# Kernel optimization log

Measured on AMD Instinct MI355X. Metric: run time of the kernel, lower is better.

## Reference

```python
import jax, jax.numpy as jnp
import numpy as np

L = 16          # hash-grid levels (opt.L)
F = 2           # features per level
N_MIN = 16      # base resolution
T = 1 << 19     # hashmap size per level (log2_T = 19, bound == 1)
BOUND = 1.0
B = float(np.exp(np.log(512.0 / 16.0) / (L - 1)))  # per-level scale
PRIMES = np.array([1, 2654435761, 805459861], dtype=np.uint32)
# 8 corner offsets of the trilinear cell, in {0,1}^3
OFFS = np.array([[i, j, k] for i in (0, 1) for j in (0, 1) for k in (0, 1)], dtype=np.float32)


def hash_grid_encode(xn, tables):
    """xn: [N,3] in [0,1]; tables: [L,T,F]. Returns [N, L*F]."""
    offs_f = jnp.asarray(OFFS)                      # [8,3] float
    offs_u = jnp.asarray(OFFS.astype(np.uint32))    # [8,3] uint32
    primes = jnp.asarray(PRIMES)
    feats = []
    for l in range(L):
        res = int(np.floor(N_MIN * B ** l))
        pos = xn * res                              # [N,3]
        pf = jnp.minimum(jnp.floor(pos), float(res - 1))
        frac = pos - pf                             # [N,3], grads flow to x
        base = pf.astype(jnp.uint32)                # [N,3]
        corners = base[:, None, :] + offs_u[None]   # [N,8,3]
        if (res + 1) ** 3 <= T:
            # grid fits in table: coherent dense indexing (tcnn behavior)
            stride = jnp.asarray(np.array([1, res + 1, (res + 1) ** 2], dtype=np.uint32))
            idx = (corners * stride).sum(-1)        # [N,8]
        else:
            h = corners * primes                    # uint32 wraps (mod 2^32)
            idx = (h[..., 0] ^ h[..., 1] ^ h[..., 2]) & jnp.uint32(T - 1)
        vals = tables[l, idx.astype(jnp.int32)]     # [N,8,F] gather
        w = jnp.prod(jnp.where(offs_f[None] > 0, frac[:, None, :], 1.0 - frac[:, None, :]), axis=-1)  # [N,8]
        feats.append(jnp.einsum('nc,ncf->nf', w, vals))
    return jnp.concatenate(feats, axis=-1)          # [N, L*F]


def _wn(v, g):
    # torch weight_norm, dim=0: per-output-row normalization
    return g[:, None] * v / jnp.linalg.norm(v, axis=1, keepdims=True)


def setup_inputs() -> dict:
    key = jax.random.key(0)
    k = jax.random.split(key, 4)
    N = 2097152
    x = jax.random.uniform(k[0], (N, 3), jnp.float32, -BOUND, BOUND)
    tables = jax.random.normal(k[1], (L, T, F), jnp.float32) * 1e-2
    v1 = jax.random.normal(k[2], (64, L * F), jnp.float32) * (1.0 / np.sqrt(L * F))
    g1 = jnp.ones((64,), jnp.float32)
    b1 = jnp.zeros((64,), jnp.float32)
    v2 = jax.random.normal(k[3], (3, 64), jnp.float32) * (1.0 / 8.0)
    g2 = jnp.ones((3,), jnp.float32)
    b2 = jnp.zeros((3,), jnp.float32)
    return {"x": x, "tables": tables, "v1": v1, "g1": g1, "b1": b1,
            "v2": v2, "g2": g2, "b2": b2}


def reference(x, tables, v1, g1, b1, v2, g2, b2):
    xn = (x + BOUND) / (2.0 * BOUND)                # map to [0,1]
    h = hash_grid_encode(xn, tables)                # [N, 32]
    h1 = jax.nn.relu(h @ _wn(v1, g1).T + b1)        # [N, 64]
    out = jnp.tanh(h1 @ _wn(v2, g2).T + b2)         # [N, 3]
    return out
```

## Files before the change

### kernel.cpp

```cpp
#include <hip/hip_runtime.h>
#include <math.h>

#define LVL 16
#define TBL (1u << 19)
#define PR1 2654435761u
#define PR2 805459861u
#define NDENSE 7
#define NHASH 9
#define NXY 5

typedef __attribute__((ext_vector_type(4))) float f4;
typedef __attribute__((ext_vector_type(4))) unsigned u4;
typedef __attribute__((ext_vector_type(8))) short bf16x8;
typedef __attribute__((ext_vector_type(4))) float f32x4;

union FragU { unsigned u[4]; bf16x8 v; };

struct EncParams {
    float resf[LVL];
    float resm1[LVL];
    unsigned s1[LVL];
    unsigned s2[LVL];
    unsigned dense_mask;
};

struct FinalParams {
    float resf[NDENSE];
    float resm1[NDENSE];
    unsigned s1[NDENSE];
    unsigned s2[NDENSE];
    unsigned off1_5, off1_6;
};

struct XYBuild { unsigned S[NXY]; unsigned s1[NXY]; };

static __device__ __forceinline__ unsigned f2bf(float f) {
    unsigned u = __float_as_uint(f);
    u += 0x7FFFu + ((u >> 16) & 1u);
    return u >> 16;
}
static __device__ __forceinline__ float bf_lo(unsigned p) { return __uint_as_float(p << 16); }
static __device__ __forceinline__ float bf_hi(unsigned p) { return __uint_as_float(p & 0xFFFF0000u); }

static __device__ __forceinline__ float fast_tanh(float v) {
    v = fminf(fmaxf(v, -10.f), 10.f);
    float e = __expf(2.0f * v);
    return __fdividef(e - 1.0f, e + 1.0f);
}

static __device__ __forceinline__ void gather8_sc0(const unsigned* __restrict__ tb,
                                                   const unsigned* off, unsigned* val)
{
    asm volatile(
        "global_load_dword %0, %8, %16 sc0\n\t"
        "global_load_dword %1, %9, %16 sc0\n\t"
        "global_load_dword %2, %10, %16 sc0\n\t"
        "global_load_dword %3, %11, %16 sc0\n\t"
        "global_load_dword %4, %12, %16 sc0\n\t"
        "global_load_dword %5, %13, %16 sc0\n\t"
        "global_load_dword %6, %14, %16 sc0\n\t"
        "global_load_dword %7, %15, %16 sc0\n\t"
        "s_waitcnt vmcnt(0)"
        : "=&v"(val[0]), "=&v"(val[1]), "=&v"(val[2]), "=&v"(val[3]),
          "=&v"(val[4]), "=&v"(val[5]), "=&v"(val[6]), "=&v"(val[7])
        : "v"(off[0]), "v"(off[1]), "v"(off[2]), "v"(off[3]),
          "v"(off[4]), "v"(off[5]), "v"(off[6]), "v"(off[7]),
          "s"(tb)
        : "memory");
}

static __device__ __forceinline__ void gather4x2_sc0(const unsigned* __restrict__ tb,
                                                     const unsigned* off,
                                                     unsigned long long* val)
{
    asm volatile(
        "global_load_dwordx2 %0, %4, %8 sc0\n\t"
        "global_load_dwordx2 %1, %5, %8 sc0\n\t"
        "global_load_dwordx2 %2, %6, %8 sc0\n\t"
        "global_load_dwordx2 %3, %7, %8 sc0\n\t"
        "s_waitcnt vmcnt(0)"
        : "=&v"(val[0]), "=&v"(val[1]), "=&v"(val[2]), "=&v"(val[3])
        : "v"(off[0]), "v"(off[1]), "v"(off[2]), "v"(off[3]),
          "s"(tb)
        : "memory");
}

static __device__ __forceinline__ void gather8x2_sc0(const unsigned* __restrict__ tb,
                                                     const unsigned* off,
                                                     unsigned long long* val)
{
    asm volatile(
        "global_load_dwordx2 %0, %8, %16 sc0\n\t"
        "global_load_dwordx2 %1, %9, %16 sc0\n\t"
        "global_load_dwordx2 %2, %10, %16 sc0\n\t"
        "global_load_dwordx2 %3, %11, %16 sc0\n\t"
        "global_load_dwordx2 %4, %12, %16 sc0\n\t"
        "global_load_dwordx2 %5, %13, %16 sc0\n\t"
        "global_load_dwordx2 %6, %14, %16 sc0\n\t"
        "global_load_dwordx2 %7, %15, %16 sc0\n\t"
        "s_waitcnt vmcnt(0)"
        : "=&v"(val[0]), "=&v"(val[1]), "=&v"(val[2]), "=&v"(val[3]),
          "=&v"(val[4]), "=&v"(val[5]), "=&v"(val[6]), "=&v"(val[7])
        : "v"(off[0]), "v"(off[1]), "v"(off[2]), "v"(off[3]),
          "v"(off[4]), "v"(off[5]), "v"(off[6]), "v"(off[7]),
          "s"(tb)
        : "memory");
}

static __device__ __forceinline__ void gather10x4_sc0(const unsigned* __restrict__ tb,
                                                      const unsigned* off, u4* val)
{
    asm volatile(
        "global_load_dwordx4 %0, %10, %20 sc0\n\t"
        "global_load_dwordx4 %1, %11, %20 sc0\n\t"
        "global_load_dwordx4 %2, %12, %20 sc0\n\t"
        "global_load_dwordx4 %3, %13, %20 sc0\n\t"
        "global_load_dwordx4 %4, %14, %20 sc0\n\t"
        "global_load_dwordx4 %5, %15, %20 sc0\n\t"
        "global_load_dwordx4 %6, %16, %20 sc0\n\t"
        "global_load_dwordx4 %7, %17, %20 sc0\n\t"
        "global_load_dwordx4 %8, %18, %20 sc0\n\t"
        "global_load_dwordx4 %9, %19, %20 sc0\n\t"
        "s_waitcnt vmcnt(0)"
        : "=&v"(val[0]), "=&v"(val[1]), "=&v"(val[2]), "=&v"(val[3]), "=&v"(val[4]),
          "=&v"(val[5]), "=&v"(val[6]), "=&v"(val[7]), "=&v"(val[8]), "=&v"(val[9])
        : "v"(off[0]), "v"(off[1]), "v"(off[2]), "v"(off[3]), "v"(off[4]),
          "v"(off[5]), "v"(off[6]), "v"(off[7]), "v"(off[8]), "v"(off[9]),
          "s"(tb)
        : "memory");
}

__global__ __launch_bounds__(256)
void prep_weights(const float* __restrict__ v1, const float* __restrict__ g1,
                  const float* __restrict__ v2, const float* __restrict__ g2,
                  float* __restrict__ ws)
{
    int t = threadIdx.x;
    if (t < 64) {
        float row[32];
        float s = 0.f;
        for (int i = 0; i < 32; ++i) { row[i] = v1[t * 32 + i]; s += row[i] * row[i]; }
        float sc = g1[t] / sqrtf(s);
        unsigned* wbf = (unsigned*)ws + 2304;
        for (int i = 0; i < 32; ++i) ws[t * 32 + i] = row[i] * sc;
        for (int w = 0; w < 16; ++w)
            wbf[t * 16 + w] = (f2bf(row[2 * w + 1] * sc) << 16) | f2bf(row[2 * w] * sc);
    } else if (t < 67) {
        int r = t - 64;
        float s = 0.f;
        for (int i = 0; i < 64; ++i) { float v = v2[r * 64 + i]; s += v * v; }
        float scale = g2[r] / sqrtf(s);
        for (int i = 0; i < 64; ++i) ws[2048 + r * 64 + i] = v2[r * 64 + i] * scale;
    }
}

__global__ __launch_bounds__(256)
void convert_tables(const float* __restrict__ src, unsigned* __restrict__ dst, int npairs)
{
    int j = blockIdx.x * 256 + threadIdx.x;
    if (j >= npairs) return;
    f4 v = __builtin_nontemporal_load((const f4*)src + j);
    unsigned lo = (f2bf(v.y) << 16) | f2bf(v.x);
    unsigned hi = (f2bf(v.w) << 16) | f2bf(v.z);
    unsigned long long o = ((unsigned long long)hi << 32) | lo;
    __builtin_nontemporal_store(o, (unsigned long long*)dst + j);
}

__global__ __launch_bounds__(256)
void build_xy(const float* __restrict__ tables, unsigned* __restrict__ region, XYBuild xb)
{
    int l = blockIdx.y;
    unsigned e = blockIdx.x * 256 + threadIdx.x;
    unsigned S = xb.S[l];
    if (e >= S) return;
    unsigned s1 = xb.s1[l];
    const float* src = tables + (size_t)l * TBL * 2;
    unsigned e10 = (e + 1u < S) ? e + 1u : e;
    unsigned e01 = (e + s1 < S) ? e + s1 : e;
    unsigned e11 = (e + s1 + 1u < S) ? e + s1 + 1u : e;
    u4 o;
    o[0] = (f2bf(src[2 * e   + 1]) << 16) | f2bf(src[2 * e]);
    o[1] = (f2bf(src[2 * e10 + 1]) << 16) | f2bf(src[2 * e10]);
    o[2] = (f2bf(src[2 * e01 + 1]) << 16) | f2bf(src[2 * e01]);
    o[3] = (f2bf(src[2 * e11 + 1]) << 16) | f2bf(src[2 * e11]);
    *(u4*)(region + (size_t)l * TBL + 4u * e) = o;
}

__global__ __launch_bounds__(256)
void build_pair1(unsigned* __restrict__ region, unsigned src_dw, unsigned dst_dw, unsigned n)
{
    unsigned e = blockIdx.x * 256 + threadIdx.x;
    if (e + 1 < n)
        region[dst_dw + e] = region[src_dw + e + 1];
}

__global__ __launch_bounds__(256, 4)
void encode_hash4(const float* __restrict__ x, const unsigned* __restrict__ tb,
                  unsigned* __restrict__ hout, int N, float rf, float rm1)
{
    int j = blockIdx.x * 256 + threadIdx.x;
    int i0 = 4 * j;
    if (i0 >= N) return;

    if (i0 + 4 <= N) {
        const f4* xp = (const f4*)(x + (size_t)3 * i0);
        f4 q0 = __builtin_nontemporal_load(xp);
        f4 q1 = __builtin_nontemporal_load(xp + 1);
        f4 q2 = __builtin_nontemporal_load(xp + 2);
        float n0[4], n1[4], n2[4];
        n0[0] = (q0.x + 1.f) * 0.5f; n1[0] = (q0.y + 1.f) * 0.5f; n2[0] = (q0.z + 1.f) * 0.5f;
        n0[1] = (q0.w + 1.f) * 0.5f; n1[1] = (q1.x + 1.f) * 0.5f; n2[1] = (q1.y + 1.f) * 0.5f;
        n0[2] = (q1.z + 1.f) * 0.5f; n1[2] = (q1.w + 1.f) * 0.5f; n2[2] = (q2.x + 1.f) * 0.5f;
        n0[3] = (q2.y + 1.f) * 0.5f; n1[3] = (q2.z + 1.f) * 0.5f; n2[3] = (q2.w + 1.f) * 0.5f;

        unsigned o[4];
#pragma unroll
        for (int p = 0; p < 4; ++p) {
            float a0 = n0[p] * rf, a1 = n1[p] * rf, a2 = n2[p] * rf;
            float w0 = fminf(floorf(a0), rm1);
            float w1 = fminf(floorf(a1), rm1);
            float w2 = fminf(floorf(a2), rm1);
            float f0 = a0 - w0, f1 = a1 - w1, f2 = a2 - w2;
            unsigned c0 = (unsigned)w0;
            unsigned hx0 = c0, hx1 = c0 + 1u;
            unsigned hy0 = (unsigned)w1 * PR1, hy1 = hy0 + PR1;
            unsigned hz0 = (unsigned)w2 * PR2, hz1 = hz0 + PR2;

            float acc0, acc1;
            if (!(c0 & 1u)) {
                unsigned pb[4], qq[4];
#pragma unroll
                for (int jj = 0; jj < 4; ++jj) {
                    unsigned hyv = (jj & 2) ? hy1 : hy0;
                    unsigned hzv = (jj & 1) ? hz1 : hz0;
                    unsigned idx0 = (hx0 ^ hyv ^ hzv) & (TBL - 1u);
                    qq[jj] = idx0 & 1u;
                    pb[jj] = (idx0 & ~1u) << 2;
                }
                unsigned long long pv[4];
                gather4x2_sc0(tb, pb, pv);
                float wx1 = f0, wx0 = 1.f - f0;
                acc0 = 0.f; acc1 = 0.f;
#pragma unroll
                for (int jj = 0; jj < 4; ++jj) {
                    unsigned lo = (unsigned)pv[jj];
                    unsigned hi = (unsigned)(pv[jj] >> 32);
                    unsigned x0 = qq[jj] ? hi : lo;
                    unsigned x1 = qq[jj] ? lo : hi;
                    float wyz = ((jj & 2) ? f1 : 1.f - f1) * ((jj & 1) ? f2 : 1.f - f2);
                    acc0 = fmaf(wyz, fmaf(wx0, bf_lo(x0), wx1 * bf_lo(x1)), acc0);
                    acc1 = fmaf(wyz, fmaf(wx0, bf_hi(x0), wx1 * bf_hi(x1)), acc1);
                }
            } else {
                unsigned off[8];
#pragma unroll
                for (int c = 0; c < 8; ++c) {
                    unsigned hx = (c & 4) ? hx1 : hx0;
                    unsigned hy = (c & 2) ? hy1 : hy0;
                    unsigned hz = (c & 1) ? hz1 : hz0;
                    off[c] = ((hx ^ hy ^ hz) & (TBL - 1u)) << 2;
                }
                unsigned v[8];
                gather8_sc0(tb, off, v);
                acc0 = 0.f; acc1 = 0.f;
#pragma unroll
                for (int c = 0; c < 8; ++c) {
                    float w = ((c & 4) ? f0 : 1.f - f0) *
                              ((c & 2) ? f1 : 1.f - f1) *
                              ((c & 1) ? f2 : 1.f - f2);
                    acc0 = fmaf(w, bf_lo(v[c]), acc0);
                    acc1 = fmaf(w, bf_hi(v[c]), acc1);
                }
            }
            o[p] = (f2bf(acc1) << 16) | f2bf(acc0);
        }
        u4 ov = {o[0], o[1], o[2], o[3]};
        __builtin_nontemporal_store(ov, (u4*)(hout + i0));
    } else {
        for (int i = i0; i < N; ++i) {
            float xn0 = (x[3 * i + 0] + 1.0f) * 0.5f;
            float xn1 = (x[3 * i + 1] + 1.0f) * 0.5f;
            float xn2 = (x[3 * i + 2] + 1.0f) * 0.5f;
            float p0 = xn0 * rf, p1 = xn1 * rf, p2 = xn2 * rf;
            float pf0 = fminf(floorf(p0), rm1), pf1 = fminf(floorf(p1), rm1), pf2 = fminf(floorf(p2), rm1);
            float fg0 = p0 - pf0, fg1 = p1 - pf1, fg2 = p2 - pf2;
            unsigned hx0 = (unsigned)pf0, hx1 = hx0 + 1u;
            unsigned hy0 = (unsigned)pf1 * PR1, hy1 = hy0 + PR1;
            unsigned hz0 = (unsigned)pf2 * PR2, hz1 = hz0 + PR2;
            float a0 = 0.f, a1 = 0.f;
#pragma unroll
            for (int c = 0; c < 8; ++c) {
                unsigned hxv = (c & 4) ? hx1 : hx0;
                unsigned hyv = (c & 2) ? hy1 : hy0;
                unsigned hzv = (c & 1) ? hz1 : hz0;
                unsigned vv = tb[(hxv ^ hyv ^ hzv) & (TBL - 1u)];
                float w = ((c & 4) ? fg0 : 1.f - fg0) * ((c & 2) ? fg1 : 1.f - fg1) * ((c & 1) ? fg2 : 1.f - fg2);
                a0 = fmaf(w, bf_lo(vv), a0);
                a1 = fmaf(w, bf_hi(vv), a1);
            }
            hout[i] = (f2bf(a1) << 16) | f2bf(a0);
        }
    }
}

__global__ __launch_bounds__(256, 4)
void final_mfma(const float* __restrict__ x, const unsigned* __restrict__ tb,
                const unsigned* __restrict__ hbuf, const unsigned* __restrict__ w1bf,
                const float* __restrict__ b1, const float* __restrict__ w2,
                const float* __restrict__ b2, float* __restrict__ out,
                int N, FinalParams dp)
{
    __shared__ unsigned lds[256 * 20];
    int tid = threadIdx.x;
    int i = blockIdx.x * 256 + tid;

    unsigned hp[NHASH];
#pragma unroll
    for (int l = 0; l < NHASH; ++l)
        hp[l] = __builtin_nontemporal_load(hbuf + (size_t)l * N + i);

    float xn0 = (__builtin_nontemporal_load(x + 3 * i + 0) + 1.0f) * 0.5f;
    float xn1 = (__builtin_nontemporal_load(x + 3 * i + 1) + 1.0f) * 0.5f;
    float xn2 = (__builtin_nontemporal_load(x + 3 * i + 2) + 1.0f) * 0.5f;

    float fr[NDENSE][3];
    unsigned bb[NDENSE];
#pragma unroll
    for (int l = 0; l < NDENSE; ++l) {
        float rf = dp.resf[l];
        float p0 = xn0 * rf, p1 = xn1 * rf, p2 = xn2 * rf;
        float pf0 = fminf(floorf(p0), dp.resm1[l]);
        float pf1 = fminf(floorf(p1), dp.resm1[l]);
        float pf2 = fminf(floorf(p2), dp.resm1[l]);
        fr[l][0] = p0 - pf0; fr[l][1] = p1 - pf1; fr[l][2] = p2 - pf2;
        bb[l] = (unsigned)pf0 + (unsigned)pf1 * dp.s1[l] + (unsigned)pf2 * dp.s2[l];
    }

    unsigned offxy[2 * NXY];
#pragma unroll
    for (int l = 0; l < NXY; ++l) {
        unsigned base = l * (TBL * 4u);
        offxy[2 * l + 0] = base + bb[l] * 16u;
        offxy[2 * l + 1] = base + (bb[l] + dp.s2[l]) * 16u;
    }
    unsigned off56[8];
#pragma unroll
    for (int h = 0; h < 2; ++h) {
        int l = 5 + h;
        unsigned base0 = l * (TBL * 4u);
        unsigned base1 = h ? dp.off1_6 : dp.off1_5;
        unsigned s1 = dp.s1[l], s2 = dp.s2[l];
#pragma unroll
        for (int jj = 0; jj < 4; ++jj) {
            unsigned e = bb[l] + ((jj & 2) ? s1 : 0u) + ((jj & 1) ? s2 : 0u);
            off56[4 * h + jj] = (e & 1u) ? (base1 + ((e - 1u) << 2)) : (base0 + (e << 2));
        }
    }

    unsigned hw[16];
    {
        u4 xv[2 * NXY];
        gather10x4_sc0(tb, offxy, xv);
#pragma unroll
        for (int l = 0; l < NXY; ++l) {
            float wx1 = fr[l][0], wx0 = 1.f - wx1;
            float wy1 = fr[l][1], wy0 = 1.f - wy1;
            float wz1 = fr[l][2];
            float acc0 = 0.f, acc1 = 0.f;
#pragma unroll
            for (int z = 0; z < 2; ++z) {
                u4 e = xv[2 * l + z];
                float wz = z ? wz1 : 1.f - wz1;
                float lo = wy0 * fmaf(wx0, bf_lo(e[0]), wx1 * bf_lo(e[1]))
                         + wy1 * fmaf(wx0, bf_lo(e[2]), wx1 * bf_lo(e[3]));
                float hi = wy0 * fmaf(wx0, bf_hi(e[0]), wx1 * bf_hi(e[1]))
                         + wy1 * fmaf(wx0, bf_hi(e[2]), wx1 * bf_hi(e[3]));
                acc0 = fmaf(wz, lo, acc0);
                acc1 = fmaf(wz, hi, acc1);
            }
            hw[l] = (f2bf(acc1) << 16) | f2bf(acc0);
        }
    }
    {
        unsigned long long pv[8];
        gather8x2_sc0(tb, off56, pv);
#pragma unroll
        for (int h = 0; h < 2; ++h) {
            int l = 5 + h;
            float wx1 = fr[l][0], wx0 = 1.f - wx1;
            float f1v = fr[l][1], f2v = fr[l][2];
            float acc0 = 0.f, acc1 = 0.f;
#pragma unroll
            for (int jj = 0; jj < 4; ++jj) {
                unsigned long long pvv = pv[4 * h + jj];
                unsigned lo = (unsigned)pvv;
                unsigned hi = (unsigned)(pvv >> 32);
                float wyz = ((jj & 2) ? f1v : 1.f - f1v) * ((jj & 1) ? f2v : 1.f - f2v);
                acc0 = fmaf(wyz, fmaf(wx0, bf_lo(lo), wx1 * bf_lo(hi)), acc0);
                acc1 = fmaf(wyz, fmaf(wx0, bf_hi(lo), wx1 * bf_hi(hi)), acc1);
            }
            hw[l] = (f2bf(acc1) << 16) | f2bf(acc0);
        }
    }
#pragma unroll
    for (int l = 0; l < NHASH; ++l) hw[NDENSE + l] = hp[l];

    unsigned* row = &lds[tid * 20];
#pragma unroll
    for (int c = 0; c < 4; ++c)
        *(uint4*)(row + 4 * c) = make_uint4(hw[4 * c], hw[4 * c + 1], hw[4 * c + 2], hw[4 * c + 3]);

    __syncthreads();

    int lane = tid & 63;
    int wv   = tid >> 6;
    int l16  = lane & 15;
    int lhi  = lane >> 4;

    bf16x8 bfr[4];
#pragma unroll
    for (int t = 0; t < 4; ++t) {
        const unsigned* p = w1bf + (t * 16 + l16) * 16 + lhi * 4;
        FragU u;
        u.u[0] = p[0]; u.u[1] = p[1]; u.u[2] = p[2]; u.u[3] = p[3];
        bfr[t] = u.v;
    }
    float b1v[4];
#pragma unroll
    for (int t = 0; t < 4; ++t) b1v[t] = b1[t * 16 + l16];
    float w2v[3][4];
#pragma unroll
    for (int jj = 0; jj < 3; ++jj)
#pragma unroll
        for (int t = 0; t < 4; ++t) w2v[jj][t] = w2[jj * 64 + t * 16 + l16];
    float bias2 = (l16 < 3) ? b2[l16] : 0.f;

#pragma unroll
    for (int g = 0; g < 4; ++g) {
        const unsigned* rp = &lds[(wv * 64 + g * 16 + l16) * 20 + lhi * 4];
        FragU u;
        u.u[0] = rp[0]; u.u[1] = rp[1]; u.u[2] = rp[2]; u.u[3] = rp[3];
        bf16x8 af = u.v;

        f32x4 acc[4];
#pragma unroll
        for (int t = 0; t < 4; ++t) {
            f32x4 z = {0.f, 0.f, 0.f, 0.f};
            acc[t] = __builtin_amdgcn_mfma_f32_16x16x32_bf16(af, bfr[t], z, 0, 0, 0);
        }

#pragma unroll
        for (int r = 0; r < 4; ++r) {
            float p0 = 0.f, p1 = 0.f, p2 = 0.f;
#pragma unroll
            for (int t = 0; t < 4; ++t) {
                float a = fmaxf(acc[t][r] + b1v[t], 0.f);
                p0 = fmaf(a, w2v[0][t], p0);
                p1 = fmaf(a, w2v[1][t], p1);
                p2 = fmaf(a, w2v[2][t], p2);
            }
#pragma unroll
            for (int m = 1; m < 16; m <<= 1) {
                p0 += __shfl_xor(p0, m);
                p1 += __shfl_xor(p1, m);
                p2 += __shfl_xor(p2, m);
            }
            if (l16 < 3) {
                int point = blockIdx.x * 256 + wv * 64 + g * 16 + lhi * 4 + r;
                float v = (l16 == 0) ? p0 : ((l16 == 1) ? p1 : p2);
                out[(size_t)point * 3 + l16] = fast_tanh(v + bias2);
            }
        }
    }
}

__global__ __launch_bounds__(256)
void fused_ngp(const float* __restrict__ x, const float* __restrict__ tables,
               const float* __restrict__ w1, const float* __restrict__ b1,
               const float* __restrict__ w2, const float* __restrict__ b2,
               float* __restrict__ out, int N, EncParams ep)
{
    int i = blockIdx.x * 256 + threadIdx.x;
    if (i >= N) return;

    float xn0 = (x[3 * i + 0] + 1.0f) * 0.5f;
    float xn1 = (x[3 * i + 1] + 1.0f) * 0.5f;
    float xn2 = (x[3 * i + 2] + 1.0f) * 0.5f;

    float h[2 * LVL];

#pragma unroll
    for (int l = 0; l < LVL; ++l) {
        float rf = ep.resf[l];
        float p0 = xn0 * rf, p1 = xn1 * rf, p2 = xn2 * rf;
        float pf0 = fminf(floorf(p0), ep.resm1[l]);
        float pf1 = fminf(floorf(p1), ep.resm1[l]);
        float pf2 = fminf(floorf(p2), ep.resm1[l]);
        float fr0 = p0 - pf0, fr1 = p1 - pf1, fr2 = p2 - pf2;
        unsigned c0 = (unsigned)pf0, c1 = (unsigned)pf1, c2 = (unsigned)pf2;
        const float2* tb = (const float2*)tables + (size_t)l * TBL;

        float acc0 = 0.f, acc1 = 0.f;
        if ((ep.dense_mask >> l) & 1u) {
            unsigned s1 = ep.s1[l], s2 = ep.s2[l];
            unsigned b = c0 + c1 * s1 + c2 * s2;
#pragma unroll
            for (int c = 0; c < 8; ++c) {
                unsigned id = b + ((c & 4) ? 1u : 0u) + ((c & 2) ? s1 : 0u) + ((c & 1) ? s2 : 0u);
                float2 v = tb[id];
                float w = ((c & 4) ? fr0 : 1.f - fr0) * ((c & 2) ? fr1 : 1.f - fr1) * ((c & 1) ? fr2 : 1.f - fr2);
                acc0 = fmaf(w, v.x, acc0);
                acc1 = fmaf(w, v.y, acc1);
            }
        } else {
            unsigned hx0 = c0, hx1 = c0 + 1u;
            unsigned hy0 = c1 * PR1, hy1 = hy0 + PR1;
            unsigned hz0 = c2 * PR2, hz1 = hz0 + PR2;
#pragma unroll
            for (int c = 0; c < 8; ++c) {
                unsigned hx = (c & 4) ? hx1 : hx0;
                unsigned hy = (c & 2) ? hy1 : hy0;
                unsigned hz = (c & 1) ? hz1 : hz0;
                float2 v = tb[(hx ^ hy ^ hz) & (TBL - 1u)];
                float w = ((c & 4) ? fr0 : 1.f - fr0) * ((c & 2) ? fr1 : 1.f - fr1) * ((c & 1) ? fr2 : 1.f - fr2);
                acc0 = fmaf(w, v.x, acc0);
                acc1 = fmaf(w, v.y, acc1);
            }
        }
        h[2 * l + 0] = acc0;
        h[2 * l + 1] = acc1;
    }

    float r0 = b2[0], r1 = b2[1], r2 = b2[2];
    for (int o = 0; o < 64; ++o) {
        float a = b1[o];
#pragma unroll
        for (int k = 0; k < 32; ++k) a = fmaf(h[k], w1[o * 32 + k], a);
        a = fmaxf(a, 0.f);
        r0 = fmaf(a, w2[0 * 64 + o], r0);
        r1 = fmaf(a, w2[1 * 64 + o], r1);
        r2 = fmaf(a, w2[2 * 64 + o], r2);
    }
    out[3 * i + 0] = tanhf(r0);
    out[3 * i + 1] = tanhf(r1);
    out[3 * i + 2] = tanhf(r2);
}

extern "C" void kernel_launch(void* const* d_in, const int* in_sizes, int n_in,
                              void* d_out, int out_size, void* d_ws, size_t ws_size,
                              hipStream_t stream)
{
    const float* x      = (const float*)d_in[0];
    const float* tables = (const float*)d_in[1];
    const float* v1     = (const float*)d_in[2];
    const float* g1     = (const float*)d_in[3];
    const float* b1     = (const float*)d_in[4];
    const float* v2     = (const float*)d_in[5];
    const float* g2     = (const float*)d_in[6];
    const float* b2     = (const float*)d_in[7];
    float* out = (float*)d_out;
    float* ws  = (float*)d_ws;
    int N = in_sizes[0] / 3;

    EncParams ep;
    double Bd = exp(log(512.0 / 16.0) / (double)(LVL - 1));
    unsigned dm = 0;
    int resv[LVL];
    for (int l = 0; l < LVL; ++l) {
        int res = (int)floor(16.0 * pow(Bd, (double)l));
        resv[l] = res;
        ep.resf[l]  = (float)res;
        ep.resm1[l] = (float)(res - 1);
        long long rp1 = (long long)res + 1;
        if (rp1 * rp1 * rp1 <= (long long)TBL) dm |= (1u << l);
        ep.s1[l] = (unsigned)(res + 1);
        ep.s2[l] = (unsigned)((res + 1) * (res + 1));
    }
    ep.dense_mask = dm;

    prep_weights<<<1, 256, 0, stream>>>(v1, g1, v2, g2, ws);

    size_t tb_off_bytes = 16384;
    unsigned S[NDENSE];
    for (int l = 0; l < NDENSE; ++l) {
        unsigned s1 = (unsigned)(resv[l] + 1);
        S[l] = s1 * s1 * s1;
    }
    bool xy_ok = true;
    for (int l = 0; l < NXY; ++l) if (4ull * S[l] > TBL) xy_ok = false;

    unsigned cum_dw = LVL * TBL;
    unsigned off1_5_dw = cum_dw; cum_dw += (S[5] + 3u) & ~1u;
    unsigned off1_6_dw = cum_dw; cum_dw += (S[6] + 3u) & ~1u;
    cum_dw = (cum_dw + 3u) & ~3u;
    size_t h_off_bytes = tb_off_bytes + (size_t)cum_dw * 4;
    size_t need = h_off_bytes + (size_t)NHASH * (size_t)N * 4;

    bool fast = (ws_size >= need) && (dm == 0x7Fu) && (N % 1024 == 0) && xy_ok;
    if (fast) {
        unsigned* tb   = (unsigned*)((char*)d_ws + tb_off_bytes);
        unsigned* hbuf = (unsigned*)((char*)d_ws + h_off_bytes);
        unsigned* w1bf = (unsigned*)ws + 2304;

        int npairs = (int)((size_t)LVL * TBL / 2);
        convert_tables<<<(npairs + 255) / 256, 256, 0, stream>>>(tables, tb, npairs);

        XYBuild xb;
        unsigned maxSxy = 0;
        for (int l = 0; l < NXY; ++l) {
            xb.S[l] = S[l]; xb.s1[l] = ep.s1[l];
            if (S[l] > maxSxy) maxSxy = S[l];
        }
        dim3 xgrid((maxSxy + 255) / 256, NXY);
        build_xy<<<xgrid, 256, 0, stream>>>(tables, tb, xb);

        build_pair1<<<(S[5] + 255) / 256, 256, 0, stream>>>(tb, 5u * TBL, off1_5_dw, S[5]);
        build_pair1<<<(S[6] + 255) / 256, 256, 0, stream>>>(tb, 6u * TBL, off1_6_dw, S[6]);

        int grid4 = N / 1024;
        for (int l = 0; l < NHASH; ++l) {
            int gl = NDENSE + l;
            encode_hash4<<<grid4, 256, 0, stream>>>(
                x, tb + (size_t)gl * TBL, hbuf + (size_t)l * N, N,
                ep.resf[gl], ep.resm1[gl]);
        }

        FinalParams dp;
        for (int l = 0; l < NDENSE; ++l) {
            dp.resf[l] = ep.resf[l]; dp.resm1[l] = ep.resm1[l];
            dp.s1[l] = ep.s1[l];     dp.s2[l] = ep.s2[l];
        }
        dp.off1_5 = off1_5_dw * 4u;
        dp.off1_6 = off1_6_dw * 4u;
        final_mfma<<<N / 256, 256, 0, stream>>>(x, tb, hbuf, w1bf, b1,
                                                ws + 2048, b2, out, N, dp);
    } else {
        fused_ngp<<<(N + 255) / 256, 256, 0, stream>>>(x, tables, ws, b1, ws + 2048, b2, out, N, ep);
    }
}
```

Baseline: 652.3 us.

## Pack all 8 trilinear corners per cell contiguously for dense levels 0-4

Replaces the xy-pair layout, which stored 4 corners per vertex and needed two strided 16-byte gathers per level, with a per-cell layout. Each cell stores all 8 bf16-packed corners in 32 contiguous bytes, so the final kernel reads two adjacent 16-byte chunks. These likely fall in the same cache line, which should cut memory transactions and cache-line traffic for the dense levels. In exchange the preprocessing build writes 32 bytes per cell, roughly twice as much as before, and the in-place xy_ok guard is removed because the cells now live in a separate workspace region.

Result: faster. 630.9 us (-3.3%).

```diff
diff --git a/kernel.cpp b/kernel.cpp
--- a/kernel.cpp
+++ b/kernel.cpp
@@ -29,10 +29,18 @@
     float resm1[NDENSE];
     unsigned s1[NDENSE];
     unsigned s2[NDENSE];
+    unsigned cellbase[NXY];
+    unsigned cres[NXY];
+    unsigned cres2[NXY];
     unsigned off1_5, off1_6;
 };
 
-struct XYBuild { unsigned S[NXY]; unsigned s1[NXY]; };
+struct CellBuild {
+    unsigned nc[NXY];
+    unsigned res[NXY];
+    unsigned s1[NXY], s2[NXY];
+    unsigned dst_dw[NXY];
+};
 
 static __device__ __forceinline__ unsigned f2bf(float f) {
     unsigned u = __float_as_uint(f);
@@ -167,23 +175,27 @@
 }
 
 __global__ __launch_bounds__(256)
-void build_xy(const float* __restrict__ tables, unsigned* __restrict__ region, XYBuild xb)
+void build_cell(const float* __restrict__ tables, unsigned* __restrict__ region, CellBuild cb)
 {
     int l = blockIdx.y;
-    unsigned e = blockIdx.x * 256 + threadIdx.x;
-    unsigned S = xb.S[l];
-    if (e >= S) return;
-    unsigned s1 = xb.s1[l];
+    unsigned c = blockIdx.x * 256 + threadIdx.x;
+    if (c >= cb.nc[l]) return;
+    unsigned res = cb.res[l];
+    unsigned cx = c % res, t = c / res;
+    unsigned cy = t % res, cz = t / res;
+    unsigned s1 = cb.s1[l], s2 = cb.s2[l];
+    unsigned base = cx + cy * s1 + cz * s2;
     const float* src = tables + (size_t)l * TBL * 2;
-    unsigned e10 = (e + 1u < S) ? e + 1u : e;
-    unsigned e01 = (e + s1 < S) ? e + s1 : e;
-    unsigned e11 = (e + s1 + 1u < S) ? e + s1 + 1u : e;
-    u4 o;
-    o[0] = (f2bf(src[2 * e   + 1]) << 16) | f2bf(src[2 * e]);
-    o[1] = (f2bf(src[2 * e10 + 1]) << 16) | f2bf(src[2 * e10]);
-    o[2] = (f2bf(src[2 * e01 + 1]) << 16) | f2bf(src[2 * e01]);
-    o[3] = (f2bf(src[2 * e11 + 1]) << 16) | f2bf(src[2 * e11]);
-    *(u4*)(region + (size_t)l * TBL + 4u * e) = o;
+    unsigned o[8];
+#pragma unroll
+    for (int k = 0; k < 8; ++k) {
+        unsigned e = base + (k & 1u) + ((k >> 1) & 1u) * s1 + (k >> 2) * s2;
+        o[k] = (f2bf(src[2 * e + 1]) << 16) | f2bf(src[2 * e]);
+    }
+    u4* dst = (u4*)(region + cb.dst_dw[l] + 8u * c);
+    u4 o0 = {o[0], o[1], o[2], o[3]};
+    u4 o1 = {o[4], o[5], o[6], o[7]};
+    dst[0] = o0; dst[1] = o1;
 }
 
 __global__ __launch_bounds__(256)
@@ -324,7 +336,7 @@
     float xn2 = (__builtin_nontemporal_load(x + 3 * i + 2) + 1.0f) * 0.5f;
 
     float fr[NDENSE][3];
-    unsigned bb[NDENSE];
+    unsigned cc[NDENSE][3];
 #pragma unroll
     for (int l = 0; l < NDENSE; ++l) {
         float rf = dp.resf[l];
@@ -333,15 +345,16 @@
         float pf1 = fminf(floorf(p1), dp.resm1[l]);
         float pf2 = fminf(floorf(p2), dp.resm1[l]);
         fr[l][0] = p0 - pf0; fr[l][1] = p1 - pf1; fr[l][2] = p2 - pf2;
-        bb[l] = (unsigned)pf0 + (unsigned)pf1 * dp.s1[l] + (unsigned)pf2 * dp.s2[l];
+        cc[l][0] = (unsigned)pf0; cc[l][1] = (unsigned)pf1; cc[l][2] = (unsigned)pf2;
     }
 
     unsigned offxy[2 * NXY];
 #pragma unroll
     for (int l = 0; l < NXY; ++l) {
-        unsigned base = l * (TBL * 4u);
-        offxy[2 * l + 0] = base + bb[l] * 16u;
-        offxy[2 * l + 1] = base + (bb[l] + dp.s2[l]) * 16u;
+        unsigned c = cc[l][0] + cc[l][1] * dp.cres[l] + cc[l][2] * dp.cres2[l];
+        unsigned base = dp.cellbase[l] + c * 32u;
+        offxy[2 * l + 0] = base;
+        offxy[2 * l + 1] = base + 16u;
     }
     unsigned off56[8];
 #pragma unroll
@@ -350,9 +363,10 @@
         unsigned base0 = l * (TBL * 4u);
         unsigned base1 = h ? dp.off1_6 : dp.off1_5;
         unsigned s1 = dp.s1[l], s2 = dp.s2[l];
+        unsigned b = cc[l][0] + cc[l][1] * s1 + cc[l][2] * s2;
 #pragma unroll
         for (int jj = 0; jj < 4; ++jj) {
-            unsigned e = bb[l] + ((jj & 2) ? s1 : 0u) + ((jj & 1) ? s2 : 0u);
+            unsigned e = b + ((jj & 2) ? s1 : 0u) + ((jj & 1) ? s2 : 0u);
             off56[4 * h + jj] = (e & 1u) ? (base1 + ((e - 1u) << 2)) : (base0 + (e << 2));
         }
     }
@@ -581,22 +595,32 @@
     prep_weights<<<1, 256, 0, stream>>>(v1, g1, v2, g2, ws);
 
     size_t tb_off_bytes = 16384;
-    unsigned S[NDENSE];
+    unsigned S[NDENSE], NC[NXY];
     for (int l = 0; l < NDENSE; ++l) {
         unsigned s1 = (unsigned)(resv[l] + 1);
         S[l] = s1 * s1 * s1;
     }
-    bool xy_ok = true;
-    for (int l = 0; l < NXY; ++l) if (4ull * S[l] > TBL) xy_ok = false;
+    for (int l = 0; l < NXY; ++l) {
+        unsigned r = (unsigned)resv[l];
+        NC[l] = r * r * r;
+    }
 
     unsigned cum_dw = LVL * TBL;
     unsigned off1_5_dw = cum_dw; cum_dw += (S[5] + 3u) & ~1u;
     unsigned off1_6_dw = cum_dw; cum_dw += (S[6] + 3u) & ~1u;
+    cum_dw = (cum_dw + 15u) & ~15u;
+    unsigned cell_dw[NXY];
+    unsigned maxNC = 0;
+    for (int l = 0; l < NXY; ++l) {
+        cell_dw[l] = cum_dw;
+        cum_dw += 8u * NC[l];
+        if (NC[l] > maxNC) maxNC = NC[l];
+    }
     cum_dw = (cum_dw + 3u) & ~3u;
     size_t h_off_bytes = tb_off_bytes + (size_t)cum_dw * 4;
     size_t need = h_off_bytes + (size_t)NHASH * (size_t)N * 4;
 
-    bool fast = (ws_size >= need) && (dm == 0x7Fu) && (N % 1024 == 0) && xy_ok;
+    bool fast = (ws_size >= need) && (dm == 0x7Fu) && (N % 1024 == 0);
     if (fast) {
         unsigned* tb   = (unsigned*)((char*)d_ws + tb_off_bytes);
         unsigned* hbuf = (unsigned*)((char*)d_ws + h_off_bytes);
@@ -605,14 +629,14 @@
         int npairs = (int)((size_t)LVL * TBL / 2);
         convert_tables<<<(npairs + 255) / 256, 256, 0, stream>>>(tables, tb, npairs);
 
-        XYBuild xb;
-        unsigned maxSxy = 0;
+        CellBuild cb;
         for (int l = 0; l < NXY; ++l) {
-            xb.S[l] = S[l]; xb.s1[l] = ep.s1[l];
-            if (S[l] > maxSxy) maxSxy = S[l];
-        }
-        dim3 xgrid((maxSxy + 255) / 256, NXY);
-        build_xy<<<xgrid, 256, 0, stream>>>(tables, tb, xb);
+            cb.nc[l] = NC[l]; cb.res[l] = (unsigned)resv[l];
+            cb.s1[l] = ep.s1[l]; cb.s2[l] = ep.s2[l];
+            cb.dst_dw[l] = cell_dw[l];
+        }
+        dim3 cgrid((maxNC + 255) / 256, NXY);
+        build_cell<<<cgrid, 256, 0, stream>>>(tables, tb, cb);
 
         build_pair1<<<(S[5] + 255) / 256, 256, 0, stream>>>(tb, 5u * TBL, off1_5_dw, S[5]);
         build_pair1<<<(S[6] + 255) / 256, 256, 0, stream>>>(tb, 6u * TBL, off1_6_dw, S[6]);
@@ -630,6 +654,11 @@
             dp.resf[l] = ep.resf[l]; dp.resm1[l] = ep.resm1[l];
             dp.s1[l] = ep.s1[l];     dp.s2[l] = ep.s2[l];
         }
+        for (int l = 0; l < NXY; ++l) {
+            dp.cellbase[l] = cell_dw[l] * 4u;
+            dp.cres[l] = (unsigned)resv[l];
+            dp.cres2[l] = (unsigned)(resv[l] * resv[l]);
+        }
         dp.off1_5 = off1_5_dw * 4u;
         dp.off1_6 = off1_6_dw * 4u;
         final_mfma<<<N / 256, 256, 0, stream>>>(x, tb, hbuf, w1bf, b1,
```
